# Optimization experiments

Measured on AMD Instinct MI355X. Metric: run time of the kernel, lower is better.

The kernel has to match this reference:

```python
import jax, jax.numpy as jnp
import numpy as np

BETA = 0.25
N_EMBED = 8192
DIM = 256


def setup_inputs() -> dict:
    key = jax.random.key(0)
    k1, k2 = jax.random.split(key)
    z = jax.random.normal(k1, (16, DIM, 32, 32), dtype=jnp.float32)
    # nn.Embedding init: uniform(-1/n_embed, 1/n_embed)
    codebook = jax.random.uniform(
        k2, (N_EMBED, DIM), dtype=jnp.float32,
        minval=-1.0 / N_EMBED, maxval=1.0 / N_EMBED)
    return {"z": z, "codebook": codebook}


def reference(z, codebook):
    # b c h w -> b h w c
    zp = jnp.transpose(z, (0, 2, 3, 1))
    b, h, w, c = zp.shape
    zf = zp.reshape(-1, c)  # [N, dim]
    # squared L2 distances: ||z||^2 + ||e||^2 - 2 z.e
    d = (jnp.sum(zf * zf, axis=1, keepdims=True)
         + jnp.sum(codebook * codebook, axis=1)
         - 2.0 * jnp.einsum('nd,kd->nk', zf, codebook))  # [N, n_embed]
    idx = jnp.argmin(d, axis=1)  # [N]
    z_q = codebook[idx].reshape(b, h, w, c)
    loss = (BETA * jnp.mean((jax.lax.stop_gradient(z_q) - zp) ** 2)
            + jnp.mean((z_q - jax.lax.stop_gradient(zp)) ** 2))
    # straight-through estimator
    z_q = zp + jax.lax.stop_gradient(z_q - zp)
    z_q = jnp.transpose(z_q, (0, 3, 1, 2))  # b h w c -> b c h w
    return z_q, loss, idx
```

## Files before the change

### kernel.cpp

```cpp
#include <hip/hip_runtime.h>
#include <cfloat>


#define NROWS 16384
#define NCODE 8192
#define DIMC  256
#define HW    1024
#define ZQN   4194304

#define ZT_OFF   0
#define CBT_OFF  2097152
#define ZSQ_OFF  3145728
#define CAND_OFF 3162112
#define SCR_OFF  3686400
#define TKT_OFF  3686402
#define LOSS_OFF ZQN
#define IDX_OFF  (ZQN + 1)

#define NSLICE 8
#define PRUNE_T 4300u
#define ZSCALE 2097152.0f

typedef __attribute__((ext_vector_type(8))) short bf16x8;
typedef __attribute__((ext_vector_type(4))) float f32x4;
typedef __attribute__((ext_vector_type(4))) unsigned int uint4v;

__device__ __forceinline__ unsigned umax(unsigned a, unsigned b) { return a > b ? a : b; }
__device__ __forceinline__ unsigned umin(unsigned a, unsigned b) { return a < b ? a : b; }

__device__ __forceinline__ unsigned short f2bf(float f) {
    unsigned u = __float_as_uint(f);
    return (unsigned short)((u + 0x7fffu + ((u >> 16) & 1u)) >> 16);
}

#define GLD_LDS16(gptr, lptr) \
  __builtin_amdgcn_global_load_lds((const __attribute__((address_space(1))) unsigned int*)(const void*)(gptr), \
                                   (__attribute__((address_space(3))) unsigned int*)(lptr), 16, 0, 0)

__global__ void prep_kernel(const float* __restrict__ z, const float* __restrict__ cb,
                            float* __restrict__ out) {
    int bid = blockIdx.x;
    int tid = threadIdx.x;
    if (bid < 1024) {
        __shared__ unsigned short lds[64 * 65];
        unsigned short* zt = (unsigned short*)(out + ZT_OFF);
        int c0 = (bid & 3) * 64;
        int n0 = (bid >> 2) * 64;
        const float* zb = z + (size_t)(n0 >> 10) * (DIMC * HW) + (n0 & 1023);
        #pragma unroll
        for (int i = 0; i < 4; ++i) {
            int f = tid + i * 256;
            int cl = f >> 4, n4 = f & 15;
            float4 v = *(const float4*)(zb + (size_t)(c0 + cl) * HW + n4 * 4);
            lds[(n4 * 4 + 0) * 65 + cl] = f2bf(v.x * ZSCALE);
            lds[(n4 * 4 + 1) * 65 + cl] = f2bf(v.y * ZSCALE);
            lds[(n4 * 4 + 2) * 65 + cl] = f2bf(v.z * ZSCALE);
            lds[(n4 * 4 + 3) * 65 + cl] = f2bf(v.w * ZSCALE);
        }
        __syncthreads();
        #pragma unroll
        for (int i = 0; i < 2; ++i) {
            int f = tid + i * 256;
            int nl = f >> 3, oct = f & 7;
            const unsigned short* p = lds + nl * 65 + oct * 8;
            uint4v u;
            u.x = (unsigned)p[0] | ((unsigned)p[1] << 16);
            u.y = (unsigned)p[2] | ((unsigned)p[3] << 16);
            u.z = (unsigned)p[4] | ((unsigned)p[5] << 16);
            u.w = (unsigned)p[6] | ((unsigned)p[7] << 16);
            *(uint4v*)(zt + (size_t)(n0 + nl) * DIMC + c0 + oct * 8) = u;
        }
    } else if (bid < 2048) {
        unsigned short* cbt = (unsigned short*)(out + CBT_OFF);
        size_t t = (size_t)(bid - 1024) * 256 + tid;
        float4 a = *(const float4*)(cb + t * 8);
        float4 b = *(const float4*)(cb + t * 8 + 4);
        uint4v u;
        u.x = (unsigned)f2bf(a.x) | ((unsigned)f2bf(a.y) << 16);
        u.y = (unsigned)f2bf(a.z) | ((unsigned)f2bf(a.w) << 16);
        u.z = (unsigned)f2bf(b.x) | ((unsigned)f2bf(b.y) << 16);
        u.w = (unsigned)f2bf(b.z) | ((unsigned)f2bf(b.w) << 16);
        *(uint4v*)(cbt + t * 8) = u;
        if (bid == 1024 && tid == 0) {
            out[LOSS_OFF] = 0.0f;
            out[SCR_OFF] = 0.0f;
            out[SCR_OFF + 1] = 0.0f;
            ((unsigned*)out)[TKT_OFF] = 0u;
        }
    } else {
        int n = (bid - 2048) * 256 + tid;
        const float* zp = z + (size_t)(n >> 10) * (DIMC * HW) + (n & 1023);
        double s = 0.0;
        for (int c = 0; c < DIMC; ++c) {
            double v = (double)zp[(size_t)c * HW];
            s += v * v;
        }
        out[ZSQ_OFF + n] = (float)s;
    }
}

__global__ __launch_bounds__(256, 2)
void argmin_kernel(float* __restrict__ out) {
    __shared__ __align__(16) unsigned short a_s[3 * 8192];
    const unsigned short* zt  = (const unsigned short*)(out + ZT_OFF);
    const unsigned short* cbt = (const unsigned short*)(out + CBT_OFF);
    unsigned* cand = (unsigned*)(out + CAND_OFF);

    int tid = threadIdx.x;
    int lane = tid & 63;
    int wv = tid >> 6;
    int col = lane & 15, qk = lane >> 4;
    int n0 = blockIdx.x * 256;
    int slice = blockIdx.y;

    bf16x8 B[4][8];
    #pragma unroll
    for (int rf = 0; rf < 4; ++rf)
        #pragma unroll
        for (int t = 0; t < 8; ++t)
            B[rf][t] = *(const bf16x8*)(zt + (size_t)(n0 + wv * 64 + rf * 16 + col) * DIMC
                                           + t * 32 + qk * 8);

    int rl2 = lane >> 5;
    int jsl = lane & 31;
    const unsigned short* srcb[4];
    #pragma unroll
    for (int c = 0; c < 4; ++c) {
        int rloc = (wv * 4 + c) * 2 + rl2;
        int src16 = jsl ^ (rloc & 7) ^ ((rloc & 8) >> 1);
        srcb[c] = cbt + ((size_t)slice * 1024 + rloc) * DIMC + src16 * 8;
    }

    unsigned U1[4] = {0, 0, 0, 0}, U2[4] = {0, 0, 0, 0};

    const unsigned sb = (unsigned)((col & 7) ^ ((col & 8) >> 1));
    const unsigned short* aoff[8];
    #pragma unroll
    for (int t = 0; t < 8; ++t)
        aoff[t] = a_s + col * 256 + (((unsigned)(qk + 4 * t)) ^ sb) * 8;

    f32x4 acc[4][2];
    const f32x4 BIASV = (f32x4){131072.0f, 131072.0f, 131072.0f, 131072.0f};

    auto stage = [&](int ch, int dsto ) {
        const size_t off = (size_t)ch * 32 * DIMC;
        unsigned short* dst = a_s + dsto;
        #pragma unroll
        for (int c = 0; c < 4; ++c)
            GLD_LDS16(srcb[c] + off, dst + (wv * 4 + c) * 512);
    };

    auto epi1 = [&](unsigned tb) {
        #pragma unroll
        for (int rf = 0; rf < 4; ++rf)
            #pragma unroll
            for (int r = 0; r < 4; ++r) {
                unsigned bits = __float_as_uint(acc[rf][1][r]);
                unsigned u = (bits & 0xFFFFFF00u) | (tb - (unsigned)(4 + r));
                unsigned lo = umin(u, U1[rf]);
                U1[rf] = umax(u, U1[rf]);
                U2[rf] = umax(lo, U2[rf]);
            }
    };

    auto compute = [&](int bufb, unsigned tb) {
        #pragma unroll
        for (int rf = 0; rf < 4; ++rf) acc[rf][0] = BIASV;
        #pragma unroll
        for (int t = 0; t < 8; ++t) {
            bf16x8 af = *(const bf16x8*)((const char*)aoff[t] + bufb);
            acc[0][0] = __builtin_amdgcn_mfma_f32_16x16x32_bf16(af, B[0][t], acc[0][0], 0, 0, 0);
            acc[1][0] = __builtin_amdgcn_mfma_f32_16x16x32_bf16(af, B[1][t], acc[1][0], 0, 0, 0);
            acc[2][0] = __builtin_amdgcn_mfma_f32_16x16x32_bf16(af, B[2][t], acc[2][0], 0, 0, 0);
            acc[3][0] = __builtin_amdgcn_mfma_f32_16x16x32_bf16(af, B[3][t], acc[3][0], 0, 0, 0);
        }
        #pragma unroll
        for (int rf = 0; rf < 4; ++rf) acc[rf][1] = BIASV;
        #pragma unroll
        for (int t = 0; t < 8; ++t) {
            bf16x8 af = *(const bf16x8*)((const char*)aoff[t] + bufb + 8192);
            acc[0][1] = __builtin_amdgcn_mfma_f32_16x16x32_bf16(af, B[0][t], acc[0][1], 0, 0, 0);
            acc[1][1] = __builtin_amdgcn_mfma_f32_16x16x32_bf16(af, B[1][t], acc[1][1], 0, 0, 0);
            acc[2][1] = __builtin_amdgcn_mfma_f32_16x16x32_bf16(af, B[2][t], acc[2][1], 0, 0, 0);
            acc[3][1] = __builtin_amdgcn_mfma_f32_16x16x32_bf16(af, B[3][t], acc[3][1], 0, 0, 0);
            {
                const int q0 = 2 * t, q1 = 2 * t + 1;
                const int rfA = q0 >> 2, rA = q0 & 3;
                const int rfB = q1 >> 2, rB = q1 & 3;
                unsigned bitsA = __float_as_uint(acc[rfA][0][rA]);
                unsigned uA = (bitsA & 0xFFFFFF00u) | (tb - (unsigned)rA);
                unsigned loA = umin(uA, U1[rfA]);
                U1[rfA] = umax(uA, U1[rfA]);
                U2[rfA] = umax(loA, U2[rfA]);
                unsigned bitsB = __float_as_uint(acc[rfB][0][rB]);
                unsigned uB = (bitsB & 0xFFFFFF00u) | (tb - (unsigned)rB);
                unsigned loB = umin(uB, U1[rfB]);
                U1[rfB] = umax(uB, U1[rfB]);
                U2[rfB] = umax(loB, U2[rfB]);
            }
        }
    };

#define CHUNK_SYNC(N)                                          \
    asm volatile("s_waitcnt vmcnt(" #N ")" ::: "memory");      \
    __builtin_amdgcn_s_barrier();                              \
    __builtin_amdgcn_sched_barrier(0);

    stage(0, 0);
    stage(1, 8192);

    CHUNK_SYNC(4)
    stage(2, 16384);
    compute(0, 255u);

    #pragma unroll 1
    for (int k = 0; k < 10; ++k) {
        const int c1 = 3 * k + 1;
        const unsigned tb = 255u - ((unsigned)c1 << 3);
        CHUNK_SYNC(4)
        stage(c1 + 2, 0);
        epi1(tb + 8u);
        compute(16384, tb);
        CHUNK_SYNC(4)
        stage(c1 + 3, 8192);
        epi1(tb);
        compute(32768, tb - 8u);
        CHUNK_SYNC(4)
        if (k < 9) stage(c1 + 4, 16384);
        epi1(tb - 8u);
        compute(0, tb - 16u);
    }
    CHUNK_SYNC(0)
    epi1(255u - (30u << 3));
    compute(16384, 255u - (31u << 3));
    epi1(255u - (31u << 3));
#undef CHUNK_SYNC

    #pragma unroll
    for (int rf = 0; rf < 4; ++rf) {
        unsigned t1 = 255u - (U1[rf] & 255u);
        unsigned c1 = (t1 >> 3) * 32 + ((t1 >> 2) & 1) * 16 + qk * 4 + (t1 & 3);
        unsigned x1 = ((((U1[rf] & 0xFFFFFF00u) - 0x47000000u) >> 3) << 10) | (1023u - c1);
        unsigned t2 = 255u - (U2[rf] & 255u);
        unsigned c2 = (t2 >> 3) * 32 + ((t2 >> 2) & 1) * 16 + qk * 4 + (t2 & 3);
        unsigned x2 = ((((U2[rf] & 0xFFFFFF00u) - 0x47000000u) >> 3) << 10) | (1023u - c2);
        unsigned p1 = __shfl_xor(x1, 16);
        unsigned p2 = __shfl_xor(x2, 16);
        unsigned s1 = umax(x1, p1), tm = umin(x1, p1);
        unsigned ym = umax(x2, p2), s4 = umin(x2, p2);
        unsigned s2 = umax(tm, ym), s3 = umin(tm, ym);
        unsigned r1 = umax(s1, __shfl_xor(s4, 32));
        unsigned r2 = umax(s2, __shfl_xor(s3, 32));
        unsigned r3 = umax(s3, __shfl_xor(s2, 32));
        unsigned r4 = umax(s4, __shfl_xor(s1, 32));
        if (qk == 0) {
            int row = wv * 64 + rf * 16 + col;
            uint4v cw; cw.x = r1; cw.y = r2; cw.z = r3; cw.w = r4;
            *(uint4v*)(cand + ((size_t)slice * NROWS + n0 + row) * 4) = cw;
        }
    }
}

__global__ __launch_bounds__(256, 4)
void fixup_kernel(const float* __restrict__ z, const float* __restrict__ cb,
                  float* __restrict__ out) {
    __shared__ float zs[32 * 264];
    __shared__ float zsq_s[32];
    __shared__ unsigned qmx[32];
    __shared__ float dsc[32 * 33];
    __shared__ unsigned cds[32 * 33];
    __shared__ unsigned bcode[32];
    __shared__ double lred[4];
    int tid = threadIdx.x;
    int n0 = blockIdx.x * 32;
    const float* zb = z + (size_t)(n0 >> 10) * (DIMC * HW) + (n0 & 1023);

    {
        int q = tid & 7, cq = tid >> 3;
        #pragma unroll
        for (int i = 0; i < 8; ++i) {
            int c = cq + i * 32;
            float4 v = *(const float4*)(zb + (size_t)c * HW + q * 4);
            int sc = c ^ (q << 2);
            zs[(q * 4 + 0) * 264 + sc] = v.x;
            zs[(q * 4 + 1) * 264 + sc] = v.y;
            zs[(q * 4 + 2) * 264 + sc] = v.z;
            zs[(q * 4 + 3) * 264 + sc] = v.w;
        }
    }
    if (tid < 32) { zsq_s[tid] = out[ZSQ_OFF + n0 + tid]; qmx[tid] = 0; }

    int j = tid >> 3, r = tid & 7;
    unsigned w[4];
    #pragma unroll
    for (int b = 0; b < 4; ++b)
        w[b] = ((const unsigned*)(out + CAND_OFF))
               [(((size_t)(j >> 2)) * NROWS + n0 + b * 8 + r) * 4 + (j & 3)];
    __syncthreads();
    #pragma unroll
    for (int b = 0; b < 4; ++b)
        atomicMax(&qmx[b * 8 + r], w[b] >> 10);
    __syncthreads();

    #pragma unroll 1
    for (int b = 0; b < 4; ++b) {
        int row = b * 8 + r;
        unsigned qv = w[b] >> 10;
        unsigned code = (unsigned)((j >> 2) * 1024) + 1023u - (w[b] & 1023u);
        bool live = (qv + PRUNE_T >= qmx[row]);
        float d = FLT_MAX;
        if (live) {
            const float* e = cb + (size_t)code * DIMC;
            const float* zrow = zs + row * 264;
            const int xr = (row >> 2) << 2;
            double a0 = 0.0, a1 = 0.0, a2 = 0.0, a3 = 0.0;
            for (int c = 0; c < DIMC; c += 16) {
                float4 e0 = *(const float4*)(e + c);
                float4 e1 = *(const float4*)(e + c + 4);
                float4 e2 = *(const float4*)(e + c + 8);
                float4 e3 = *(const float4*)(e + c + 12);
                float4 z0 = *(const float4*)(zrow + ((c) ^ xr));
                float4 z1 = *(const float4*)(zrow + ((c + 4) ^ xr));
                float4 z2 = *(const float4*)(zrow + ((c + 8) ^ xr));
                float4 z3 = *(const float4*)(zrow + ((c + 12) ^ xr));
                a0 += (double)z0.x * (double)e0.x + (double)z0.y * (double)e0.y
                    + (double)z0.z * (double)e0.z + (double)z0.w * (double)e0.w;
                a1 += (double)z1.x * (double)e1.x + (double)z1.y * (double)e1.y
                    + (double)z1.z * (double)e1.z + (double)z1.w * (double)e1.w;
                a2 += (double)z2.x * (double)e2.x + (double)z2.y * (double)e2.y
                    + (double)z2.z * (double)e2.z + (double)z2.w * (double)e2.w;
                a3 += (double)z3.x * (double)e3.x + (double)z3.y * (double)e3.y
                    + (double)z3.z * (double)e3.z + (double)z3.w * (double)e3.w;
            }
            d = fmaf(-2.0f, (float)((a0 + a1) + (a2 + a3)), zsq_s[row]);
        }
        dsc[row * 33 + j] = d;
        cds[row * 33 + j] = code;
    }
    __syncthreads();
    if (tid < 32) {
        float bd = FLT_MAX; unsigned bi = 0xffffffffu;
        for (int jj = 0; jj < 32; ++jj) {
            float dv = dsc[tid * 33 + jj];
            unsigned k = cds[tid * 33 + jj];
            if (dv < bd || (dv == bd && k < bi)) { bd = dv; bi = k; }
        }
        out[IDX_OFF + n0 + tid] = (float)bi;
        bcode[tid] = bi;
    }
    __syncthreads();

    {
        int row = tid & 31, cg = tid >> 5;
        const float* zrow = zs + row * 264;
        const int xr = (row >> 2) << 2;
        const float* e = cb + (size_t)bcode[row] * DIMC;
        double lacc = 0.0;
        #pragma unroll
        for (int i = 0; i < 8; ++i) {
            int c = cg * 32 + (((i + row) & 7) << 2);
            float4 ev = *(const float4*)(e + c);
            float4 zv = *(const float4*)(zrow + (c ^ xr));
            double d0 = (double)ev.x - (double)zv.x;
            double d1 = (double)ev.y - (double)zv.y;
            double d2 = (double)ev.z - (double)zv.z;
            double d3 = (double)ev.w - (double)zv.w;
            lacc += d0 * d0 + d1 * d1 + d2 * d2 + d3 * d3;
        }
        #pragma unroll
        for (int off = 32; off; off >>= 1) lacc += __shfl_down(lacc, off);
        if ((tid & 63) == 0) lred[tid >> 6] = lacc;
    }
    __syncthreads();
    if (tid == 0) {
        double part = (lred[0] + lred[1]) + (lred[2] + lred[3]);
        atomicAdd((double*)(out + SCR_OFF), part);
        asm volatile("s_waitcnt vmcnt(0)" ::: "memory");
        unsigned t = atomicAdd(((unsigned*)out) + TKT_OFF, 1u);
        if (t == 511u) {
            double tot = atomicAdd((double*)(out + SCR_OFF), 0.0);
            out[LOSS_OFF] = (float)(tot * (1.25 / 4194304.0));
        }
    }
}

__global__ __launch_bounds__(256)
void zq_kernel(const float* __restrict__ z, const float* __restrict__ cb,
               float* __restrict__ out) {
    __shared__ float lds[16 * 260];
    int tid = threadIdx.x;
    int n0 = blockIdx.x * 16;
    {
        int rr = tid >> 4, q = tid & 15;
        int code = (int)out[IDX_OFF + n0 + rr];
        const float* e = cb + (size_t)code * DIMC;
        #pragma unroll
        for (int jj = 0; jj < 4; ++jj) {
            int c = q * 4 + jj * 64;
            *(float4*)(lds + rr * 260 + c) = *(const float4*)(e + c);
        }
    }
    __syncthreads();
    int g = tid >> 2, rq = tid & 3;
    int b = n0 >> 10, hw0 = n0 & 1023;
    const size_t base = (size_t)b * (DIMC * HW) + hw0 + rq * 4;
    #pragma unroll
    for (int i = 0; i < 4; ++i) {
        int c = g + i * 64;
        float4 v;
        v.x = lds[(rq * 4 + 0) * 260 + c];
        v.y = lds[(rq * 4 + 1) * 260 + c];
        v.z = lds[(rq * 4 + 2) * 260 + c];
        v.w = lds[(rq * 4 + 3) * 260 + c];
        *(float4*)(out + base + (size_t)c * HW) = v;
    }
}

extern "C" void kernel_launch(void* const* d_in, const int* in_sizes, int n_in,
                              void* d_out, int out_size, void* d_ws, size_t ws_size,
                              hipStream_t stream) {
    const float* z  = (const float*)d_in[0];
    const float* cb = (const float*)d_in[1];
    float* out = (float*)d_out;

    prep_kernel<<<2112, 256, 0, stream>>>(z, cb, out);
    argmin_kernel<<<dim3(64, NSLICE), 256, 0, stream>>>(out);
    fixup_kernel<<<512, 256, 0, stream>>>(z, cb, out);
    zq_kernel<<<1024, 256, 0, stream>>>(z, cb, out);
}
```

Before: 185.9 us.

## Split codebook into more slices, double-buffer LDS, simplify loss reduction

The argmin kernel now splits the codebook into 16 slices of 512 codes instead of 8 of 1024. It drops from triple- to double-buffered LDS staging with plain __syncthreads in place of counted waits, and raises the occupancy hint to 4 blocks per CU to get more parallelism. The fixup kernel now merges 64 candidates per row, and it reuses the index output area to hold the squared norms temporarily. The double-precision loss accumulation with a ticket-based final write is replaced by a direct float atomicAdd, which removes the extra atomics but makes the loss summation order-dependent and less precise. The fixup kernel also gets more per-row work, and its occupancy hint is lowered.

```diff
diff --git a/kernel.cpp b/kernel.cpp
--- a/kernel.cpp
+++ b/kernel.cpp
@@ -10,14 +10,11 @@
 
 #define ZT_OFF   0
 #define CBT_OFF  2097152
-#define ZSQ_OFF  3145728
-#define CAND_OFF 3162112
-#define SCR_OFF  3686400
-#define TKT_OFF  3686402
+#define CAND_OFF 3145728
 #define LOSS_OFF ZQN
 #define IDX_OFF  (ZQN + 1)
 
-#define NSLICE 8
+#define NSLICE 16
 #define PRUNE_T 4300u
 #define ZSCALE 2097152.0f
 
@@ -81,12 +78,7 @@
         u.z = (unsigned)f2bf(b.x) | ((unsigned)f2bf(b.y) << 16);
         u.w = (unsigned)f2bf(b.z) | ((unsigned)f2bf(b.w) << 16);
         *(uint4v*)(cbt + t * 8) = u;
-        if (bid == 1024 && tid == 0) {
-            out[LOSS_OFF] = 0.0f;
-            out[SCR_OFF] = 0.0f;
-            out[SCR_OFF + 1] = 0.0f;
-            ((unsigned*)out)[TKT_OFF] = 0u;
-        }
+        if (bid == 1024 && tid == 0) out[LOSS_OFF] = 0.0f;
     } else {
         int n = (bid - 2048) * 256 + tid;
         const float* zp = z + (size_t)(n >> 10) * (DIMC * HW) + (n & 1023);
@@ -95,13 +87,13 @@
             double v = (double)zp[(size_t)c * HW];
             s += v * v;
         }
-        out[ZSQ_OFF + n] = (float)s;
-    }
-}
-
-__global__ __launch_bounds__(256, 2)
+        out[IDX_OFF + n] = (float)s;
+    }
+}
+
+__global__ __launch_bounds__(256, 4)
 void argmin_kernel(float* __restrict__ out) {
-    __shared__ __align__(16) unsigned short a_s[3 * 8192];
+    __shared__ __align__(16) unsigned short a_s[2 * 8192];
     const unsigned short* zt  = (const unsigned short*)(out + ZT_OFF);
     const unsigned short* cbt = (const unsigned short*)(out + CBT_OFF);
     unsigned* cand = (unsigned*)(out + CAND_OFF);
@@ -128,7 +120,7 @@
     for (int c = 0; c < 4; ++c) {
         int rloc = (wv * 4 + c) * 2 + rl2;
         int src16 = jsl ^ (rloc & 7) ^ ((rloc & 8) >> 1);
-        srcb[c] = cbt + ((size_t)slice * 1024 + rloc) * DIMC + src16 * 8;
+        srcb[c] = cbt + ((size_t)slice * 512 + rloc) * DIMC + src16 * 8;
     }
 
     unsigned U1[4] = {0, 0, 0, 0}, U2[4] = {0, 0, 0, 0};
@@ -163,7 +155,7 @@
             }
     };
 
-    auto compute = [&](int bufb, unsigned tb) {
+    auto compute = [&](int bufb , unsigned tb) {
         #pragma unroll
         for (int rf = 0; rf < 4; ++rf) acc[rf][0] = BIASV;
         #pragma unroll
@@ -201,40 +193,28 @@
         }
     };
 
-#define CHUNK_SYNC(N)                                          \
-    asm volatile("s_waitcnt vmcnt(" #N ")" ::: "memory");      \
-    __builtin_amdgcn_s_barrier();                              \
-    __builtin_amdgcn_sched_barrier(0);
-
     stage(0, 0);
+    __syncthreads();
     stage(1, 8192);
-
-    CHUNK_SYNC(4)
-    stage(2, 16384);
     compute(0, 255u);
 
     #pragma unroll 1
-    for (int k = 0; k < 10; ++k) {
-        const int c1 = 3 * k + 1;
+    for (int k = 0; k < 7; ++k) {
+        const int c1 = 2 * k + 1;
         const unsigned tb = 255u - ((unsigned)c1 << 3);
-        CHUNK_SYNC(4)
-        stage(c1 + 2, 0);
+        __syncthreads();
+        stage(c1 + 1, 0);
         epi1(tb + 8u);
         compute(16384, tb);
-        CHUNK_SYNC(4)
-        stage(c1 + 3, 8192);
+        __syncthreads();
+        stage(c1 + 2, 8192);
         epi1(tb);
-        compute(32768, tb - 8u);
-        CHUNK_SYNC(4)
-        if (k < 9) stage(c1 + 4, 16384);
-        epi1(tb - 8u);
-        compute(0, tb - 16u);
-    }
-    CHUNK_SYNC(0)
-    epi1(255u - (30u << 3));
-    compute(16384, 255u - (31u << 3));
-    epi1(255u - (31u << 3));
-#undef CHUNK_SYNC
+        compute(0, tb - 8u);
+    }
+    __syncthreads();
+    epi1(255u - (14u << 3));
+    compute(16384, 255u - (15u << 3));
+    epi1(255u - (15u << 3));
 
     #pragma unroll
     for (int rf = 0; rf < 4; ++rf) {
@@ -261,14 +241,14 @@
     }
 }
 
-__global__ __launch_bounds__(256, 4)
+__global__ __launch_bounds__(256, 2)
 void fixup_kernel(const float* __restrict__ z, const float* __restrict__ cb,
                   float* __restrict__ out) {
     __shared__ float zs[32 * 264];
     __shared__ float zsq_s[32];
     __shared__ unsigned qmx[32];
-    __shared__ float dsc[32 * 33];
-    __shared__ unsigned cds[32 * 33];
+    __shared__ float dsc[32 * 65];
+    __shared__ unsigned cds[32 * 65];
     __shared__ unsigned bcode[32];
     __shared__ double lred[4];
     int tid = threadIdx.x;
@@ -288,25 +268,30 @@
             zs[(q * 4 + 3) * 264 + sc] = v.w;
         }
     }
-    if (tid < 32) { zsq_s[tid] = out[ZSQ_OFF + n0 + tid]; qmx[tid] = 0; }
+    if (tid < 32) { zsq_s[tid] = out[IDX_OFF + n0 + tid]; qmx[tid] = 0; }
 
     int j = tid >> 3, r = tid & 7;
-    unsigned w[4];
-    #pragma unroll
-    for (int b = 0; b < 4; ++b)
-        w[b] = ((const unsigned*)(out + CAND_OFF))
-               [(((size_t)(j >> 2)) * NROWS + n0 + b * 8 + r) * 4 + (j & 3)];
-    __syncthreads();
-    #pragma unroll
-    for (int b = 0; b < 4; ++b)
-        atomicMax(&qmx[b * 8 + r], w[b] >> 10);
+    unsigned w[2][4];
+    #pragma unroll
+    for (int h = 0; h < 2; ++h)
+        #pragma unroll
+        for (int b = 0; b < 4; ++b)
+            w[h][b] = ((const unsigned*)(out + CAND_OFF))
+                      [(((size_t)(h * 8 + (j >> 2))) * NROWS + n0 + b * 8 + r) * 4 + (j & 3)];
+    __syncthreads();
+    #pragma unroll
+    for (int h = 0; h < 2; ++h)
+        #pragma unroll
+        for (int b = 0; b < 4; ++b)
+            atomicMax(&qmx[b * 8 + r], w[h][b] >> 10);
     __syncthreads();
 
     #pragma unroll 1
-    for (int b = 0; b < 4; ++b) {
+    for (int hb = 0; hb < 8; ++hb) {
+        int h = hb >> 2, b = hb & 3;
         int row = b * 8 + r;
-        unsigned qv = w[b] >> 10;
-        unsigned code = (unsigned)((j >> 2) * 1024) + 1023u - (w[b] & 1023u);
+        unsigned qv = w[h][b] >> 10;
+        unsigned code = (unsigned)((h * 8 + (j >> 2)) * 512) + 1023u - (w[h][b] & 1023u);
         bool live = (qv + PRUNE_T >= qmx[row]);
         float d = FLT_MAX;
         if (live) {
@@ -334,15 +319,15 @@
             }
             d = fmaf(-2.0f, (float)((a0 + a1) + (a2 + a3)), zsq_s[row]);
         }
-        dsc[row * 33 + j] = d;
-        cds[row * 33 + j] = code;
+        dsc[row * 65 + h * 32 + j] = d;
+        cds[row * 65 + h * 32 + j] = code;
     }
     __syncthreads();
     if (tid < 32) {
         float bd = FLT_MAX; unsigned bi = 0xffffffffu;
-        for (int jj = 0; jj < 32; ++jj) {
-            float dv = dsc[tid * 33 + jj];
-            unsigned k = cds[tid * 33 + jj];
+        for (int jj = 0; jj < 64; ++jj) {
+            float dv = dsc[tid * 65 + jj];
+            unsigned k = cds[tid * 65 + jj];
             if (dv < bd || (dv == bd && k < bi)) { bd = dv; bi = k; }
         }
         out[IDX_OFF + n0 + tid] = (float)bi;
@@ -374,13 +359,7 @@
     __syncthreads();
     if (tid == 0) {
         double part = (lred[0] + lred[1]) + (lred[2] + lred[3]);
-        atomicAdd((double*)(out + SCR_OFF), part);
-        asm volatile("s_waitcnt vmcnt(0)" ::: "memory");
-        unsigned t = atomicAdd(((unsigned*)out) + TKT_OFF, 1u);
-        if (t == 511u) {
-            double tot = atomicAdd((double*)(out + SCR_OFF), 0.0);
-            out[LOSS_OFF] = (float)(tot * (1.25 / 4194304.0));
-        }
+        atomicAdd(out + LOSS_OFF, (float)(part * (1.25 / 4194304.0)));
     }
 }
 
```

Result: slower. 590.3 us (+217.5%).
